# Optimization experiments

Measured on AMD Instinct MI355X. Metric: run time of the kernel, lower is better.

Reference implementation:

```python
import jax, jax.numpy as jnp
import numpy as np

N_STATE = 4      # d_state from CrossMambaFusionBlock(d_state=4)
DT_RANK = 48     # ceil(768/16), standard Mamba dt_rank='auto'
D_CONV = 4       # depthwise causal conv kernel size


def _ln(x, g, b):
    m = jnp.mean(x, axis=-1, keepdims=True)
    v = jnp.mean((x - m) ** 2, axis=-1, keepdims=True)
    return (x - m) * jax.lax.rsqrt(v + 1e-5) * g + b


def _dwconv1d(u, w, b):
    # u: (B,L,D); w: (D,1,K) depthwise causal conv along token dim L
    K = w.shape[-1]
    up = jnp.pad(jnp.transpose(u, (0, 2, 1)), ((0, 0), (0, 0), (K - 1, 0)))
    out = jax.lax.conv_general_dilated(up, w, (1,), 'VALID',
                                       feature_group_count=w.shape[0],
                                       dimension_numbers=('NCH', 'OIH', 'NCH'))
    return jnp.transpose(out, (0, 2, 1)) + b


def _pre(x, g, b, Win, Wconv, bconv, Wxp, Wdt, bdt):
    # LayerNorm -> in_proj -> depthwise conv + SiLU -> dt/B/C projections
    B_, H, W, C = x.shape
    xn = _ln(x, g, b).reshape(B_, H * W, C)
    u, z = jnp.split(xn @ Win, 2, axis=-1)              # (B,L,D) each
    u = jax.nn.silu(_dwconv1d(u, Wconv, bconv))
    dbl = u @ Wxp                                        # (B,L,R+2N)
    dtr, Bm, Cm = jnp.split(dbl, [DT_RANK, DT_RANK + N_STATE], axis=-1)
    dt = jax.nn.softplus(dtr @ Wdt + bdt)                # (B,L,D)
    return u, z, dt, Bm, Cm


def _selective_scan(u, dt, Alog, Bm, Cm, Dskip):
    # u, dt: (B,L,D); Alog: (D,N); Bm, Cm: (B,L,N)
    A = -jnp.exp(Alog)
    dA = jnp.exp(dt[..., None] * A)                      # (B,L,D,N) decay
    dBu = (dt * u)[..., None] * Bm[:, :, None, :]        # (B,L,D,N) input

    def comb(c1, c2):
        a1, h1 = c1
        a2, h2 = c2
        return a1 * a2, a2 * h1 + h2

    _, h = jax.lax.associative_scan(comb, (dA, dBu), axis=1)
    return jnp.einsum('bldn,bln->bld', h, Cm) + u * Dskip


def _forward(x1, x2,
             ln_g1, ln_b1, Win1, Wconv1, bconv1, Wxp1, Wdt1, bdt1, Alog1, Dskip1, Wout1,
             ln_g2, ln_b2, Win2, Wconv2, bconv2, Wxp2, Wdt2, bdt2, Alog2, Dskip2, Wout2):
    x1 = jnp.transpose(x1, (0, 2, 3, 1))  # BCHW -> BHWC (as in forward_features)
    x2 = jnp.transpose(x2, (0, 2, 3, 1))
    B_, H, W, C = x1.shape
    u1, z1, dt1, B1, C1 = _pre(x1, ln_g1, ln_b1, Win1, Wconv1, bconv1, Wxp1, Wdt1, bdt1)
    u2, z2, dt2, B2, C2 = _pre(x2, ln_g2, ln_b2, Win2, Wconv2, bconv2, Wxp2, Wdt2, bdt2)
    # Cross-modal fusion: each stream's SSM state is read out with the OTHER
    # stream's C projection (cross selective scan).
    y1 = _selective_scan(u1, dt1, Alog1, B1, C2, Dskip1)
    y2 = _selective_scan(u2, dt2, Alog2, B2, C1, Dskip2)
    o1 = ((y1 * jax.nn.silu(z1)) @ Wout1).reshape(B_, H, W, C)
    o2 = ((y2 * jax.nn.silu(z2)) @ Wout2).reshape(B_, H, W, C)
    return x1 + o1, x2 + o2


def setup_inputs():
    key = jax.random.key(0)
    ks = jax.random.split(key, 16)
    B_, C, H, W = 2, 768, 64, 64
    D = C  # d_inner (ssm_ratio = 1)

    def nrm(k, shape, s=0.02):
        return jax.random.normal(k, shape, jnp.float32) * s

    inp = {
        'x1': jax.random.normal(ks[0], (B_, C, H, W), jnp.float32),
        'x2': jax.random.normal(ks[1], (B_, C, H, W), jnp.float32),
    }
    for i, o in ((1, 2), (2, 8)):
        inp[f'ln_g{i}'] = jnp.ones((C,), jnp.float32)
        inp[f'ln_b{i}'] = jnp.zeros((C,), jnp.float32)
        inp[f'Win{i}'] = nrm(ks[o], (C, 2 * D))
        inp[f'Wconv{i}'] = nrm(ks[o + 1], (D, 1, D_CONV), 0.1)
        inp[f'bconv{i}'] = jnp.zeros((D,), jnp.float32)
        inp[f'Wxp{i}'] = nrm(ks[o + 2], (D, DT_RANK + 2 * N_STATE))
        inp[f'Wdt{i}'] = nrm(ks[o + 3], (DT_RANK, D), 0.05)
        inp[f'bdt{i}'] = jnp.full((D,), -4.6, jnp.float32)  # softplus -> dt ~ 0.01
        inp[f'Alog{i}'] = jnp.log(jnp.broadcast_to(
            jnp.arange(1, N_STATE + 1, dtype=jnp.float32), (D, N_STATE)))
        inp[f'Dskip{i}'] = jnp.ones((D,), jnp.float32)
        inp[f'Wout{i}'] = nrm(ks[o + 4], (D, C))
    return inp


def reference(x1, x2,
              ln_g1, ln_b1, Win1, Wconv1, bconv1, Wxp1, Wdt1, bdt1, Alog1, Dskip1, Wout1,
              ln_g2, ln_b2, Win2, Wconv2, bconv2, Wxp2, Wdt2, bdt2, Alog2, Dskip2, Wout2):
    return _forward(x1, x2,
                    ln_g1, ln_b1, Win1, Wconv1, bconv1, Wxp1, Wdt1, bdt1, Alog1, Dskip1, Wout1,
                    ln_g2, ln_b2, Win2, Wconv2, bconv2, Wxp2, Wdt2, bdt2, Alog2, Dskip2, Wout2)
```

## Files before the change

kernel.cpp:

```cpp
#include <hip/hip_runtime.h>
#include <cmath>

#define LDIM 4096
#define CDIM 768
#define BDIM 2
#define NST 4
#define RNK 48
#define CH 64
#define LC 64
#define NDT 1024

typedef short bf16x8 __attribute__((ext_vector_type(8)));
typedef float f32x4 __attribute__((ext_vector_type(4)));

__device__ __forceinline__ float sigmoidf_(float x) { return 1.f / (1.f + __expf(-x)); }

__device__ __forceinline__ unsigned short f2bf(float f) {
    unsigned int u = __float_as_uint(f);
    u += 0x7fffu + ((u >> 16) & 1u);
    return (unsigned short)(u >> 16);
}
__device__ __forceinline__ float bf2f(unsigned short us) {
    unsigned int u = ((unsigned int)us) << 16;
    return __uint_as_float(u);
}

__device__ __forceinline__ void llds16(const unsigned short* g, unsigned short* l) {
    __builtin_amdgcn_global_load_lds(
        (const __attribute__((address_space(1))) unsigned int*)g,
        (__attribute__((address_space(3))) unsigned int*)l, 16, 0, 0);
}

__global__ __launch_bounds__(256) void stats_kernel(const float* __restrict__ x0,
                                                    const float* __restrict__ x1,
                                                    float* __restrict__ stats)
{
    int blk = blockIdx.x;
    int s = blk >> 7;
    int b = (blk >> 6) & 1;
    int l0 = (blk & 63) * 64;
    int wave = threadIdx.x >> 6, lane = threadIdx.x & 63;
    const float* x = s ? x1 : x0;
    const float* xp = x + ((size_t)b * CDIM) * LDIM + l0 + lane;
    float sm = 0.f, sq = 0.f;
    int cbeg = wave * 192;
#pragma unroll
    for (int i0 = 0; i0 < 192; i0 += 16) {
        float v[16];
#pragma unroll
        for (int j = 0; j < 16; j++) v[j] = xp[(size_t)(cbeg + i0 + j) * LDIM];
#pragma unroll
        for (int j = 0; j < 16; j++) { sm += v[j]; sq += v[j] * v[j]; }
    }
    __shared__ float red[2][4][64];
    red[0][wave][lane] = sm;
    red[1][wave][lane] = sq;
    __syncthreads();
    if (wave == 0) {
        float s_ = red[0][0][lane] + red[0][1][lane] + red[0][2][lane] + red[0][3][lane];
        float q_ = red[1][0][lane] + red[1][1][lane] + red[1][2][lane] + red[1][3][lane];
        float m = s_ * (1.f / CDIM);
        float var = q_ * (1.f / CDIM) - m * m;
        int idx = s * 8192 + b * LDIM + l0 + lane;
        stats[2 * idx] = m;
        stats[2 * idx + 1] = rsqrtf(var + 1e-5f);
    }
}

__global__ __launch_bounds__(256) void transpose_ln_kernel(
    const float* __restrict__ x0, const float* __restrict__ x1,
    const float* __restrict__ g0, const float* __restrict__ bb0,
    const float* __restrict__ g1, const float* __restrict__ bb1,
    const float* __restrict__ stats,
    unsigned short* __restrict__ xnb0, unsigned short* __restrict__ xnb1,
    float* __restrict__ out)
{
    __shared__ float tile[64][65];
    int t = threadIdx.x;
    int c0 = blockIdx.x * 64, l0 = blockIdx.y * 64;
    int z = blockIdx.z;
    int s = z >> 1, b = z & 1;
    const float* x = s ? x1 : x0;
    const float* g = s ? g1 : g0;
    const float* bb = s ? bb1 : bb0;
    unsigned short* xnb = s ? xnb1 : xnb0;
    int tl = t & 63, tg = t >> 6;
#pragma unroll
    for (int i = 0; i < 16; i++) {
        int cl = tg * 16 + i;
        tile[cl][tl] = x[((size_t)(b * CDIM + c0 + cl)) * LDIM + l0 + tl];
    }
    __syncthreads();
    const size_t SZ = (size_t)BDIM * LDIM * CDIM;
#pragma unroll
    for (int i = 0; i < 16; i++) {
        int ll = tg * 16 + i;
        int l = l0 + ll, c = c0 + tl;
        float v = tile[tl][ll];
        int sidx = s * 8192 + b * LDIM + l;
        float m = stats[sidx * 2], rs = stats[sidx * 2 + 1];
        size_t o = ((size_t)(b * LDIM + l)) * CDIM + c;
        out[(size_t)s * SZ + o] = v;
        xnb[o] = f2bf((v - m) * rs * g[c] + bb[c]);
    }
}

__global__ __launch_bounds__(256) void wt_transpose_all(
    const float* __restrict__ Win0, const float* __restrict__ Win1,
    const float* __restrict__ Wout0, const float* __restrict__ Wout1,
    unsigned short* __restrict__ WinT0, unsigned short* __restrict__ WinT1,
    unsigned short* __restrict__ WoutT0, unsigned short* __restrict__ WoutT1)
{
    int z = blockIdx.z;
    const float* W = (z == 0) ? Win0 : (z == 1) ? Win1 : (z == 2) ? Wout0 : Wout1;
    unsigned short* Wt = (z == 0) ? WinT0 : (z == 1) ? WinT1 : (z == 2) ? WoutT0 : WoutT1;
    const int K = CDIM;
    const int N = (z < 2) ? 2 * CDIM : CDIM;
    if (blockIdx.x * 64 >= N) return;
    __shared__ float tile[64][65];
    int t = threadIdx.x;
    int n0 = blockIdx.x * 64, k0 = blockIdx.y * 64;
    int tn = t & 63, tg = t >> 6;
#pragma unroll
    for (int i = 0; i < 16; i++) {
        int kl = tg * 16 + i;
        tile[kl][tn] = W[(size_t)(k0 + kl) * N + n0 + tn];
    }
    __syncthreads();
#pragma unroll
    for (int i = 0; i < 16; i++) {
        int nl = tg * 16 + i;
        int k = k0 + tn, n = n0 + nl;
        Wt[(size_t)n * K + k] = f2bf(tile[tn][nl]);
    }
}

__global__ __launch_bounds__(256) void wcomb_kernel(
    const float* __restrict__ Wxp0, const float* __restrict__ Wdt0,
    const float* __restrict__ Wxp1, const float* __restrict__ Wdt1,
    unsigned short* __restrict__ W0, unsigned short* __restrict__ W1)
{
    int s = blockIdx.z;
    const float* Wxp = s ? Wxp1 : Wxp0;
    const float* Wdt = s ? Wdt1 : Wdt0;
    unsigned short* WcombT = s ? W1 : W0;
    int t = threadIdx.x;
    int k = blockIdx.x * 64 + (t & 63);
    int n0 = blockIdx.y * 64;
    float wx[RNK];
#pragma unroll
    for (int r = 0; r < RNK; r++) wx[r] = Wxp[k * 56 + r];
    for (int i = (t >> 6); i < 64; i += 4) {
        int n = n0 + i;
        float val;
        if (n < CDIM) {
            float acc = 0.f;
#pragma unroll
            for (int r = 0; r < RNK; r++) acc += wx[r] * Wdt[(size_t)r * CDIM + n];
            val = acc;
        } else if (n < CDIM + 8) {
            val = Wxp[k * 56 + RNK + (n - CDIM)];
        } else {
            val = 0.f;
        }
        WcombT[(size_t)n * CDIM + k] = f2bf(val);
    }
}

template <int NW>
__global__ __launch_bounds__(512, 2) void gemm_mfma(
    const unsigned short* __restrict__ A0, const unsigned short* __restrict__ A1,
    const unsigned short* __restrict__ Bt0, const unsigned short* __restrict__ Bt1,
    void* __restrict__ C0, void* __restrict__ C1, int ldc, int K, int epi,
    const float* __restrict__ bias0, const float* __restrict__ bias1,
    float* __restrict__ D0, float* __restrict__ D1)
{
    const unsigned short* A = blockIdx.z ? A1 : A0;
    const unsigned short* Bt = blockIdx.z ? Bt1 : Bt0;
    void* C = blockIdx.z ? C1 : C0;
    const float* bias = blockIdx.z ? bias1 : bias0;
    float* D = blockIdx.z ? D1 : D0;

    constexpr int BN = NW * 64;
    __shared__ unsigned short As[2][256 * 64];
    __shared__ unsigned short Bs[2][BN * 64];

    const int tid = threadIdx.x;
    const int wave = tid >> 6, lane = tid & 63;
    const int row0 = blockIdx.x * 256, col0 = blockIdx.y * BN;
    const int wm = (wave >> 2) * 128;
    const int wn = (wave & 3) * (NW * 16);
    f32x4 acc[8][NW] = {};

    const int rs = tid >> 3;
    const int kcg = (tid & 7) ^ (rs & 7);
    const unsigned short* gA = A + (size_t)(row0 + rs) * K + kcg * 8;
    const unsigned short* gB = Bt + (size_t)(col0 + rs) * K + kcg * 8;
    const size_t rK = (size_t)64 * K;
    const int fr = lane & 15, fc = lane >> 4;

    auto ldfrag = [&](const unsigned short* s, int row, int kc) -> bf16x8 {
        return *(const bf16x8*)&s[row * 64 + ((kc ^ (row & 7)) << 3)];
    };

#define GSTAGE(nb, kt)                                                  \
    do {                                                                \
        const unsigned short* a_ = gA + (size_t)(kt) * 64;              \
        const unsigned short* b_ = gB + (size_t)(kt) * 64;              \
        unsigned short* al = &As[nb][wave * 512];                       \
        unsigned short* bl = &Bs[nb][wave * 512];                       \
        _Pragma("unroll")                                               \
        for (int r_ = 0; r_ < 4; r_++) llds16(a_ + r_ * rK, al + r_ * 4096); \
        _Pragma("unroll")                                               \
        for (int r_ = 0; r_ < NW; r_++) llds16(b_ + r_ * rK, bl + r_ * 4096); \
    } while (0)

    const int NKT = K / 64;
    GSTAGE(0, 0);
    __builtin_amdgcn_s_waitcnt(0xF70);
    __builtin_amdgcn_s_barrier();

    for (int kt = 0; kt < NKT; kt++) {
        const int cur = kt & 1;
        const unsigned short* as = As[cur];
        const unsigned short* bs = Bs[cur];
        bf16x8 af[4], bfv[NW];

        if (kt + 1 < NKT) GSTAGE(cur ^ 1, kt + 1);
#pragma unroll
        for (int mi = 0; mi < 4; mi++) af[mi] = ldfrag(as, wm + mi * 16 + fr, fc);
#pragma unroll
        for (int nj = 0; nj < NW; nj++) bfv[nj] = ldfrag(bs, wn + nj * 16 + fr, fc);
        __builtin_amdgcn_s_barrier();
        __builtin_amdgcn_s_setprio(1);
#pragma unroll
        for (int mi = 0; mi < 4; mi++)
#pragma unroll
            for (int nj = 0; nj < NW; nj++)
                acc[mi][nj] = __builtin_amdgcn_mfma_f32_16x16x32_bf16(af[mi], bfv[nj], acc[mi][nj], 0, 0, 0);
        __builtin_amdgcn_s_setprio(0);
        __builtin_amdgcn_s_barrier();

#pragma unroll
        for (int mi = 0; mi < 4; mi++) af[mi] = ldfrag(as, wm + 64 + mi * 16 + fr, fc);
        __builtin_amdgcn_s_barrier();
        __builtin_amdgcn_s_setprio(1);
#pragma unroll
        for (int mi = 0; mi < 4; mi++)
#pragma unroll
            for (int nj = 0; nj < NW; nj++)
                acc[4 + mi][nj] = __builtin_amdgcn_mfma_f32_16x16x32_bf16(af[mi], bfv[nj], acc[4 + mi][nj], 0, 0, 0);
        __builtin_amdgcn_s_setprio(0);
        __builtin_amdgcn_s_barrier();

#pragma unroll
        for (int mi = 0; mi < 4; mi++) af[mi] = ldfrag(as, wm + mi * 16 + fr, 4 + fc);
#pragma unroll
        for (int nj = 0; nj < NW; nj++) bfv[nj] = ldfrag(bs, wn + nj * 16 + fr, 4 + fc);
        __builtin_amdgcn_s_barrier();
        __builtin_amdgcn_s_setprio(1);
#pragma unroll
        for (int mi = 0; mi < 4; mi++)
#pragma unroll
            for (int nj = 0; nj < NW; nj++)
                acc[mi][nj] = __builtin_amdgcn_mfma_f32_16x16x32_bf16(af[mi], bfv[nj], acc[mi][nj], 0, 0, 0);
        __builtin_amdgcn_s_setprio(0);
        __builtin_amdgcn_s_barrier();

#pragma unroll
        for (int mi = 0; mi < 4; mi++) af[mi] = ldfrag(as, wm + 64 + mi * 16 + fr, 4 + fc);
        __builtin_amdgcn_s_barrier();
        __builtin_amdgcn_s_setprio(1);
#pragma unroll
        for (int mi = 0; mi < 4; mi++)
#pragma unroll
            for (int nj = 0; nj < NW; nj++)
                acc[4 + mi][nj] = __builtin_amdgcn_mfma_f32_16x16x32_bf16(af[mi], bfv[nj], acc[4 + mi][nj], 0, 0, 0);
        __builtin_amdgcn_s_setprio(0);
        if (kt + 1 < NKT) __builtin_amdgcn_s_waitcnt(0xF70);
        __builtin_amdgcn_s_barrier();
    }
#undef GSTAGE

    const int cr = (lane >> 4) * 4, cc = lane & 15;
#pragma unroll
    for (int mi = 0; mi < 8; mi++)
#pragma unroll
        for (int nj = 0; nj < NW; nj++) {
            int col = col0 + wn + nj * 16 + cc;
#pragma unroll
            for (int r = 0; r < 4; r++) {
                int row = row0 + wm + mi * 16 + cr + r;
                float v = acc[mi][nj][r];
                if (epi == 1) {
                    float* Cf = (float*)C;
                    size_t o = (size_t)row * ldc + col;
                    Cf[o] = v + Cf[o];
                } else if (epi == 2) {
                    if (col < CDIM) {
                        v += bias[col];
                        v = (v > 20.f) ? v : __logf(1.f + __expf(v));
                        ((unsigned short*)C)[(size_t)row * ldc + col] = f2bf(v);
                    } else if (col < CDIM + 8) {
                        D[(size_t)row * 8 + (col - CDIM)] = v;
                    }
                } else {
                    ((unsigned short*)C)[(size_t)row * ldc + col] = f2bf(v);
                }
            }
        }
}

__global__ __launch_bounds__(256) void conv_silu_kernel(
    const unsigned short* __restrict__ uzb0, const unsigned short* __restrict__ uzb1,
    const float* __restrict__ w0, const float* __restrict__ bc0,
    const float* __restrict__ w1, const float* __restrict__ bc1,
    unsigned short* __restrict__ ub0, unsigned short* __restrict__ ub1)
{
    int s = blockIdx.y;
    const unsigned short* uzb = s ? uzb1 : uzb0;
    const float* w = s ? w1 : w0;
    const float* bc = s ? bc1 : bc0;
    unsigned short* ub = s ? ub1 : ub0;
    int idx = blockIdx.x * 256 + threadIdx.x;
    int d8 = (idx % 96) * 8;
    int bl = idx / 96;
    int l = bl & (LDIM - 1);

    float wr[8][4];
#pragma unroll
    for (int q = 0; q < 8; q++) {
        f32x4 wv = *(const f32x4*)&w[(d8 + q) * 4];
#pragma unroll
        for (int k = 0; k < 4; k++) wr[q][k] = wv[k];
    }
    float acc[8];
    f32x4 b0 = *(const f32x4*)&bc[d8];
    f32x4 b1 = *(const f32x4*)&bc[d8 + 4];
#pragma unroll
    for (int q = 0; q < 4; q++) { acc[q] = b0[q]; acc[4 + q] = b1[q]; }

#pragma unroll
    for (int k = 0; k < 4; k++) {
        int ls = l - 3 + k;
        if (ls >= 0) {
            bf16x8 uv = *(const bf16x8*)&uzb[(size_t)(bl - 3 + k) * (2 * CDIM) + d8];
#pragma unroll
            for (int q = 0; q < 8; q++)
                acc[q] += bf2f((unsigned short)uv[q]) * wr[q][k];
        }
    }
    bf16x8 ov;
#pragma unroll
    for (int q = 0; q < 8; q++) {
        float v = acc[q];
        ov[q] = (short)f2bf(v * sigmoidf_(v));
    }
    *(bf16x8*)&ub[(size_t)bl * CDIM + d8] = ov;
}

__global__ __launch_bounds__(256) void scan_phaseA(
    const unsigned short* __restrict__ u0, const unsigned short* __restrict__ dt0,
    const float* __restrict__ dbl0, const float* __restrict__ Alog0,
    const unsigned short* __restrict__ u1, const unsigned short* __restrict__ dt1,
    const float* __restrict__ dbl1, const float* __restrict__ Alog1,
    float* __restrict__ agg)
{
    int idx = blockIdx.x * 256 + threadIdx.x;
    int d = idx % CDIM;
    int t1 = idx / CDIM;
    int c = t1 % CH;
    int t2 = t1 / CH;
    int b = t2 & 1;
    int s = t2 >> 1;
    const unsigned short* u = s ? u1 : u0;
    const unsigned short* dt = s ? dt1 : dt0;
    const float* dbl = s ? dbl1 : dbl0;
    const float* Alog = s ? Alog1 : Alog0;
    float A[4];
#pragma unroll
    for (int n = 0; n < 4; n++) A[n] = -__expf(Alog[d * 4 + n]);
    float h[4] = {0, 0, 0, 0}, aa[4] = {1, 1, 1, 1};
    int rowb = b * LDIM + c * LC;
    for (int t = 0; t < LC; t++) {
        int row = rowb + t;
        float dtv = bf2f(dt[(size_t)row * CDIM + d]);
        float uv = bf2f(u[(size_t)row * CDIM + d]);
        float du = dtv * uv;
        const float* bm = dbl + (size_t)row * 8;
#pragma unroll
        for (int n = 0; n < 4; n++) {
            float dA = __expf(dtv * A[n]);
            h[n] = dA * h[n] + du * bm[n];
            aa[n] *= dA;
        }
    }
    float* o = agg + (size_t)idx * 8;
#pragma unroll
    for (int n = 0; n < 4; n++) { o[n] = aa[n]; o[4 + n] = h[n]; }
}

__global__ __launch_bounds__(256) void scan_phaseB(const float* __restrict__ agg,
                                                   float* __restrict__ hinit)
{
    int idx = blockIdx.x * 256 + threadIdx.x;
    int d = idx % CDIM;
    int sb = idx / CDIM;
    float st[4] = {0, 0, 0, 0};
    for (int c = 0; c < CH; c++) {
        size_t base = ((size_t)sb * CH + c) * CDIM + d;
        const float* a = agg + base * 8;
        float* hi = hinit + base * 4;
#pragma unroll
        for (int n = 0; n < 4; n++) hi[n] = st[n];
#pragma unroll
        for (int n = 0; n < 4; n++) st[n] = a[n] * st[n] + a[4 + n];
    }
}

__global__ __launch_bounds__(256) void scan_phaseC(
    const unsigned short* __restrict__ u0, const unsigned short* __restrict__ dt0,
    const unsigned short* __restrict__ uzb0, const float* __restrict__ dbl0,
    const float* __restrict__ Alog0, const float* __restrict__ Dsk0, unsigned short* __restrict__ g0,
    const unsigned short* __restrict__ u1, const unsigned short* __restrict__ dt1,
    const unsigned short* __restrict__ uzb1, const float* __restrict__ dbl1,
    const float* __restrict__ Alog1, const float* __restrict__ Dsk1, unsigned short* __restrict__ g1,
    const float* __restrict__ hinit)
{
    int idx = blockIdx.x * 256 + threadIdx.x;
    int d = idx % CDIM;
    int t1 = idx / CDIM;
    int c = t1 % CH;
    int t2 = t1 / CH;
    int b = t2 & 1;
    int s = t2 >> 1;
    const unsigned short* u = s ? u1 : u0;
    const unsigned short* dt = s ? dt1 : dt0;
    const unsigned short* uzb = s ? uzb1 : uzb0;
    const float* dbl = s ? dbl1 : dbl0;
    const float* dblO = s ? dbl0 : dbl1;
    const float* Alog = s ? Alog1 : Alog0;
    const float* Dsk = s ? Dsk1 : Dsk0;
    unsigned short* gated = s ? g1 : g0;
    float A[4];
#pragma unroll
    for (int n = 0; n < 4; n++) A[n] = -__expf(Alog[d * 4 + n]);
    float Dv = Dsk[d];
    float h[4];
    const float* hi = hinit + (size_t)idx * 4;
#pragma unroll
    for (int n = 0; n < 4; n++) h[n] = hi[n];
    int rowb = b * LDIM + c * LC;
    for (int t = 0; t < LC; t++) {
        int row = rowb + t;
        float dtv = bf2f(dt[(size_t)row * CDIM + d]);
        float uv = bf2f(u[(size_t)row * CDIM + d]);
        float du = dtv * uv;
        const float* bm = dbl + (size_t)row * 8;
        const float* cm = dblO + (size_t)row * 8 + 4;
        float y = 0.f;
#pragma unroll
        for (int n = 0; n < 4; n++) {
            float dA = __expf(dtv * A[n]);
            h[n] = dA * h[n] + du * bm[n];
            y += h[n] * cm[n];
        }
        y += uv * Dv;
        float zv = bf2f(uzb[(size_t)row * (2 * CDIM) + CDIM + d]);
        gated[(size_t)row * CDIM + d] = f2bf(y * (zv * sigmoidf_(zv)));
    }
}

extern "C" void kernel_launch(void* const* d_in, const int* in_sizes, int n_in,
                              void* d_out, int out_size, void* d_ws, size_t ws_size,
                              hipStream_t stream)
{
    const float* x[2] = {(const float*)d_in[0], (const float*)d_in[1]};
    const float *ln_g[2], *ln_b[2], *Win[2], *Wconv[2], *bconv[2], *Wxp[2],
        *Wdt[2], *bdt[2], *Alog[2], *Dskip[2], *Wout[2];
    for (int s = 0; s < 2; s++) {
        int base = 2 + s * 11;
        ln_g[s] = (const float*)d_in[base + 0];
        ln_b[s] = (const float*)d_in[base + 1];
        Win[s] = (const float*)d_in[base + 2];
        Wconv[s] = (const float*)d_in[base + 3];
        bconv[s] = (const float*)d_in[base + 4];
        Wxp[s] = (const float*)d_in[base + 5];
        Wdt[s] = (const float*)d_in[base + 6];
        bdt[s] = (const float*)d_in[base + 7];
        Alog[s] = (const float*)d_in[base + 8];
        Dskip[s] = (const float*)d_in[base + 9];
        Wout[s] = (const float*)d_in[base + 10];
    }

    const int M = BDIM * LDIM;
    char* base = (char*)d_ws;
    auto alloc = [&](size_t bytes) {
        char* p = base;
        base += (bytes + 255) & ~(size_t)255;
        return p;
    };
    unsigned short* uzb[2] = {(unsigned short*)alloc((size_t)M * 1536 * 2),
                              (unsigned short*)alloc((size_t)M * 1536 * 2)};
    unsigned short* dtb[2] = {(unsigned short*)alloc((size_t)M * CDIM * 2),
                              (unsigned short*)alloc((size_t)M * CDIM * 2)};
    unsigned short* ub[2] = {(unsigned short*)alloc((size_t)M * CDIM * 2),
                             (unsigned short*)alloc((size_t)M * CDIM * 2)};
    unsigned short* xnb[2] = {(unsigned short*)alloc((size_t)M * CDIM * 2),
                              (unsigned short*)alloc((size_t)M * CDIM * 2)};
    float* dbl[2] = {(float*)alloc((size_t)M * 8 * 4), (float*)alloc((size_t)M * 8 * 4)};
    unsigned short* WinT[2] = {(unsigned short*)alloc(1536 * 768 * 2),
                               (unsigned short*)alloc(1536 * 768 * 2)};
    unsigned short* WoutT[2] = {(unsigned short*)alloc(768 * 768 * 2),
                                (unsigned short*)alloc(768 * 768 * 2)};
    unsigned short* WcombT[2] = {(unsigned short*)alloc((size_t)NDT * 768 * 2),
                                 (unsigned short*)alloc((size_t)NDT * 768 * 2)};
    float* agg = (float*)alloc((size_t)2 * BDIM * CH * CDIM * 8 * 4);
    float* hinit = (float*)alloc((size_t)2 * BDIM * CH * CDIM * 4 * 4);
    float* stats = (float*)alloc((size_t)2 * M * 2 * 4);

    dim3 blk(256);
    dim3 blk512(512);
    const size_t SZ = (size_t)BDIM * LDIM * CDIM;

    stats_kernel<<<dim3(256), blk, 0, stream>>>(x[0], x[1], stats);
    transpose_ln_kernel<<<dim3(CDIM / 64, LDIM / 64, 4), blk, 0, stream>>>(
        x[0], x[1], ln_g[0], ln_b[0], ln_g[1], ln_b[1], stats, xnb[0], xnb[1], (float*)d_out);

    wt_transpose_all<<<dim3(1536 / 64, 768 / 64, 4), blk, 0, stream>>>(
        Win[0], Win[1], Wout[0], Wout[1], WinT[0], WinT[1], WoutT[0], WoutT[1]);
    wcomb_kernel<<<dim3(768 / 64, NDT / 64, 2), blk, 0, stream>>>(
        Wxp[0], Wdt[0], Wxp[1], Wdt[1], WcombT[0], WcombT[1]);

    gemm_mfma<3><<<dim3(M / 256, 1536 / 192, 2), blk512, 0, stream>>>(
        xnb[0], xnb[1], WinT[0], WinT[1], uzb[0], uzb[1], 2 * CDIM, CDIM, 3,
        nullptr, nullptr, nullptr, nullptr);

    conv_silu_kernel<<<dim3((M * CDIM / 8) / 256, 2), blk, 0, stream>>>(
        uzb[0], uzb[1], Wconv[0], bconv[0], Wconv[1], bconv[1], ub[0], ub[1]);

    gemm_mfma<4><<<dim3(M / 256, NDT / 256, 2), blk512, 0, stream>>>(
        ub[0], ub[1], WcombT[0], WcombT[1], dtb[0], dtb[1], CDIM, CDIM, 2,
        bdt[0], bdt[1], dbl[0], dbl[1]);

    scan_phaseA<<<dim3((2 * BDIM * CH * CDIM) / 256), blk, 0, stream>>>(
        ub[0], dtb[0], dbl[0], Alog[0], ub[1], dtb[1], dbl[1], Alog[1], agg);
    scan_phaseB<<<dim3((2 * BDIM * CDIM) / 256), blk, 0, stream>>>(agg, hinit);
    scan_phaseC<<<dim3((2 * BDIM * CH * CDIM) / 256), blk, 0, stream>>>(
        ub[0], dtb[0], uzb[0], dbl[0], Alog[0], Dskip[0], xnb[0],
        ub[1], dtb[1], uzb[1], dbl[1], Alog[1], Dskip[1], xnb[1], hinit);

    float* out = (float*)d_out;
    gemm_mfma<3><<<dim3(M / 256, CDIM / 192, 2), blk512, 0, stream>>>(
        xnb[0], xnb[1], WoutT[0], WoutT[1], out, out + SZ, CDIM, CDIM, 1,
        nullptr, nullptr, nullptr, nullptr);
}
```

Before: 490.1 us.

## Merge prep kernels, retile GEMM to 256x128, trim dt padding, vectorize LN loads

Merges the stats, weight-transpose and weight-combine kernels into one launch, which saves launch overhead. Replaces the templated GEMM, which had a 256xNW*64 tile and a barrier/setprio ping-pong schedule, with a fixed 256x128 tile using a 4x4 MFMA fragment per wave and a simpler loop with one barrier per k-step. The combined dt weight padding drops from 1024 to 896 columns, cutting wasted GEMM work. The LayerNorm transpose now loads input with float4 vectors. The simpler GEMM schedule may lose latency hiding and the smaller N tile reduces reuse of A.

After: 475.3 us. -3.0%, faster.

```diff
diff --git a/kernel.cpp b/kernel.cpp
--- a/kernel.cpp
+++ b/kernel.cpp
@@ -8,7 +8,7 @@
 #define RNK 48
 #define CH 64
 #define LC 64
-#define NDT 1024
+#define NDT 896
 
 typedef short bf16x8 __attribute__((ext_vector_type(8)));
 typedef float f32x4 __attribute__((ext_vector_type(4)));
@@ -31,39 +31,103 @@
         (__attribute__((address_space(3))) unsigned int*)l, 16, 0, 0);
 }
 
-__global__ __launch_bounds__(256) void stats_kernel(const float* __restrict__ x0,
-                                                    const float* __restrict__ x1,
-                                                    float* __restrict__ stats)
-{
-    int blk = blockIdx.x;
-    int s = blk >> 7;
-    int b = (blk >> 6) & 1;
-    int l0 = (blk & 63) * 64;
-    int wave = threadIdx.x >> 6, lane = threadIdx.x & 63;
-    const float* x = s ? x1 : x0;
-    const float* xp = x + ((size_t)b * CDIM) * LDIM + l0 + lane;
-    float sm = 0.f, sq = 0.f;
-    int cbeg = wave * 192;
-#pragma unroll
-    for (int i0 = 0; i0 < 192; i0 += 16) {
-        float v[16];
-#pragma unroll
-        for (int j = 0; j < 16; j++) v[j] = xp[(size_t)(cbeg + i0 + j) * LDIM];
-#pragma unroll
-        for (int j = 0; j < 16; j++) { sm += v[j]; sq += v[j] * v[j]; }
-    }
-    __shared__ float red[2][4][64];
-    red[0][wave][lane] = sm;
-    red[1][wave][lane] = sq;
-    __syncthreads();
-    if (wave == 0) {
-        float s_ = red[0][0][lane] + red[0][1][lane] + red[0][2][lane] + red[0][3][lane];
-        float q_ = red[1][0][lane] + red[1][1][lane] + red[1][2][lane] + red[1][3][lane];
-        float m = s_ * (1.f / CDIM);
-        float var = q_ * (1.f / CDIM) - m * m;
-        int idx = s * 8192 + b * LDIM + l0 + lane;
-        stats[2 * idx] = m;
-        stats[2 * idx + 1] = rsqrtf(var + 1e-5f);
+__global__ __launch_bounds__(256) void prep_kernel(
+    const float* __restrict__ x0, const float* __restrict__ x1, float* __restrict__ stats,
+    const float* __restrict__ Win0, const float* __restrict__ Win1,
+    const float* __restrict__ Wout0, const float* __restrict__ Wout1,
+    unsigned short* __restrict__ WinT0, unsigned short* __restrict__ WinT1,
+    unsigned short* __restrict__ WoutT0, unsigned short* __restrict__ WoutT1,
+    const float* __restrict__ Wxp0, const float* __restrict__ Wdt0,
+    const float* __restrict__ Wxp1, const float* __restrict__ Wdt1,
+    unsigned short* __restrict__ Wc0, unsigned short* __restrict__ Wc1)
+{
+    __shared__ float smem[64 * 65];
+    int bid = blockIdx.x;
+    int t = threadIdx.x;
+
+    if (bid < 256) {
+        int s = bid >> 7;
+        int b = (bid >> 6) & 1;
+        int l0 = (bid & 63) * 64;
+        int wave = t >> 6, lane = t & 63;
+        const float* x = s ? x1 : x0;
+        const float* xp = x + ((size_t)b * CDIM) * LDIM + l0 + lane;
+        float sm = 0.f, sq = 0.f;
+        int cbeg = wave * 192;
+#pragma unroll
+        for (int i0 = 0; i0 < 192; i0 += 16) {
+            float v[16];
+#pragma unroll
+            for (int j = 0; j < 16; j++) v[j] = xp[(size_t)(cbeg + i0 + j) * LDIM];
+#pragma unroll
+            for (int j = 0; j < 16; j++) { sm += v[j]; sq += v[j] * v[j]; }
+        }
+        float* red = smem;
+        red[(0 * 4 + wave) * 64 + lane] = sm;
+        red[(1 * 4 + wave) * 64 + lane] = sq;
+        __syncthreads();
+        if (wave == 0) {
+            float s_ = red[lane] + red[64 + lane] + red[128 + lane] + red[192 + lane];
+            float q_ = red[256 + lane] + red[320 + lane] + red[384 + lane] + red[448 + lane];
+            float m = s_ * (1.f / CDIM);
+            float var = q_ * (1.f / CDIM) - m * m;
+            int idx = s * 8192 + b * LDIM + l0 + lane;
+            stats[2 * idx] = m;
+            stats[2 * idx + 1] = rsqrtf(var + 1e-5f);
+        }
+        return;
+    }
+    if (bid < 1408) {
+        int b2 = bid - 256;
+        int bx = b2 % 24, by = (b2 / 24) % 12, z = b2 / 288;
+        const float* W = (z == 0) ? Win0 : (z == 1) ? Win1 : (z == 2) ? Wout0 : Wout1;
+        unsigned short* Wt = (z == 0) ? WinT0 : (z == 1) ? WinT1 : (z == 2) ? WoutT0 : WoutT1;
+        const int K = CDIM;
+        const int N = (z < 2) ? 2 * CDIM : CDIM;
+        if (bx * 64 >= N) return;
+        float (*tile)[65] = (float(*)[65])smem;
+        int n0 = bx * 64, k0 = by * 64;
+        int tn = t & 63, tg = t >> 6;
+#pragma unroll
+        for (int i = 0; i < 16; i++) {
+            int kl = tg * 16 + i;
+            tile[kl][tn] = W[(size_t)(k0 + kl) * N + n0 + tn];
+        }
+        __syncthreads();
+#pragma unroll
+        for (int i = 0; i < 16; i++) {
+            int nl = tg * 16 + i;
+            int k = k0 + tn, n = n0 + nl;
+            Wt[(size_t)n * K + k] = f2bf(tile[tn][nl]);
+        }
+        return;
+    }
+    {
+        int b3 = bid - 1408;
+        int bx = b3 % 12, by = (b3 / 12) % 14, s = b3 / 168;
+        const float* Wxp = s ? Wxp1 : Wxp0;
+        const float* Wdt = s ? Wdt1 : Wdt0;
+        unsigned short* WcombT = s ? Wc1 : Wc0;
+        int k = bx * 64 + (t & 63);
+        int n0 = by * 64;
+        float wx[RNK];
+#pragma unroll
+        for (int r = 0; r < RNK; r++) wx[r] = Wxp[k * 56 + r];
+        for (int i = (t >> 6); i < 64; i += 4) {
+            int n = n0 + i;
+            float val;
+            if (n < CDIM) {
+                float acc = 0.f;
+#pragma unroll
+                for (int r = 0; r < RNK; r++) acc += wx[r] * Wdt[(size_t)r * CDIM + n];
+                val = acc;
+            } else if (n < CDIM + 8) {
+                val = Wxp[k * 56 + RNK + (n - CDIM)];
+            } else {
+                val = 0.f;
+            }
+            WcombT[(size_t)n * CDIM + k] = f2bf(val);
+        }
     }
 }
 
@@ -84,14 +148,17 @@
     const float* g = s ? g1 : g0;
     const float* bb = s ? bb1 : bb0;
     unsigned short* xnb = s ? xnb1 : xnb0;
-    int tl = t & 63, tg = t >> 6;
-#pragma unroll
-    for (int i = 0; i < 16; i++) {
-        int cl = tg * 16 + i;
-        tile[cl][tl] = x[((size_t)(b * CDIM + c0 + cl)) * LDIM + l0 + tl];
+    int lane16 = t & 15, cg = t >> 4;
+#pragma unroll
+    for (int i = 0; i < 4; i++) {
+        int cl = cg + 16 * i;
+        f32x4 v = *(const f32x4*)&x[((size_t)(b * CDIM + c0 + cl)) * LDIM + l0 + lane16 * 4];
+#pragma unroll
+        for (int j = 0; j < 4; j++) tile[cl][lane16 * 4 + j] = v[j];
     }
     __syncthreads();
     const size_t SZ = (size_t)BDIM * LDIM * CDIM;
+    int tl = t & 63, tg = t >> 6;
 #pragma unroll
     for (int i = 0; i < 16; i++) {
         int ll = tg * 16 + i;
@@ -105,69 +172,6 @@
     }
 }
 
-__global__ __launch_bounds__(256) void wt_transpose_all(
-    const float* __restrict__ Win0, const float* __restrict__ Win1,
-    const float* __restrict__ Wout0, const float* __restrict__ Wout1,
-    unsigned short* __restrict__ WinT0, unsigned short* __restrict__ WinT1,
-    unsigned short* __restrict__ WoutT0, unsigned short* __restrict__ WoutT1)
-{
-    int z = blockIdx.z;
-    const float* W = (z == 0) ? Win0 : (z == 1) ? Win1 : (z == 2) ? Wout0 : Wout1;
-    unsigned short* Wt = (z == 0) ? WinT0 : (z == 1) ? WinT1 : (z == 2) ? WoutT0 : WoutT1;
-    const int K = CDIM;
-    const int N = (z < 2) ? 2 * CDIM : CDIM;
-    if (blockIdx.x * 64 >= N) return;
-    __shared__ float tile[64][65];
-    int t = threadIdx.x;
-    int n0 = blockIdx.x * 64, k0 = blockIdx.y * 64;
-    int tn = t & 63, tg = t >> 6;
-#pragma unroll
-    for (int i = 0; i < 16; i++) {
-        int kl = tg * 16 + i;
-        tile[kl][tn] = W[(size_t)(k0 + kl) * N + n0 + tn];
-    }
-    __syncthreads();
-#pragma unroll
-    for (int i = 0; i < 16; i++) {
-        int nl = tg * 16 + i;
-        int k = k0 + tn, n = n0 + nl;
-        Wt[(size_t)n * K + k] = f2bf(tile[tn][nl]);
-    }
-}
-
-__global__ __launch_bounds__(256) void wcomb_kernel(
-    const float* __restrict__ Wxp0, const float* __restrict__ Wdt0,
-    const float* __restrict__ Wxp1, const float* __restrict__ Wdt1,
-    unsigned short* __restrict__ W0, unsigned short* __restrict__ W1)
-{
-    int s = blockIdx.z;
-    const float* Wxp = s ? Wxp1 : Wxp0;
-    const float* Wdt = s ? Wdt1 : Wdt0;
-    unsigned short* WcombT = s ? W1 : W0;
-    int t = threadIdx.x;
-    int k = blockIdx.x * 64 + (t & 63);
-    int n0 = blockIdx.y * 64;
-    float wx[RNK];
-#pragma unroll
-    for (int r = 0; r < RNK; r++) wx[r] = Wxp[k * 56 + r];
-    for (int i = (t >> 6); i < 64; i += 4) {
-        int n = n0 + i;
-        float val;
-        if (n < CDIM) {
-            float acc = 0.f;
-#pragma unroll
-            for (int r = 0; r < RNK; r++) acc += wx[r] * Wdt[(size_t)r * CDIM + n];
-            val = acc;
-        } else if (n < CDIM + 8) {
-            val = Wxp[k * 56 + RNK + (n - CDIM)];
-        } else {
-            val = 0.f;
-        }
-        WcombT[(size_t)n * CDIM + k] = f2bf(val);
-    }
-}
-
-template <int NW>
 __global__ __launch_bounds__(512, 2) void gemm_mfma(
     const unsigned short* __restrict__ A0, const unsigned short* __restrict__ A1,
     const unsigned short* __restrict__ Bt0, const unsigned short* __restrict__ Bt1,
@@ -181,16 +185,15 @@
     const float* bias = blockIdx.z ? bias1 : bias0;
     float* D = blockIdx.z ? D1 : D0;
 
-    constexpr int BN = NW * 64;
     __shared__ unsigned short As[2][256 * 64];
-    __shared__ unsigned short Bs[2][BN * 64];
+    __shared__ unsigned short Bs[2][128 * 64];
 
     const int tid = threadIdx.x;
     const int wave = tid >> 6, lane = tid & 63;
-    const int row0 = blockIdx.x * 256, col0 = blockIdx.y * BN;
-    const int wm = (wave >> 2) * 128;
-    const int wn = (wave & 3) * (NW * 16);
-    f32x4 acc[8][NW] = {};
+    const int row0 = blockIdx.x * 256, col0 = blockIdx.y * 128;
+    const int wm = (wave >> 1) * 64;
+    const int wn = (wave & 1) * 64;
+    f32x4 acc[4][4] = {};
 
     const int rs = tid >> 3;
     const int kcg = (tid & 7) ^ (rs & 7);
@@ -203,16 +206,16 @@
         return *(const bf16x8*)&s[row * 64 + ((kc ^ (row & 7)) << 3)];
     };
 
-#define GSTAGE(nb, kt)                                                  \
-    do {                                                                \
-        const unsigned short* a_ = gA + (size_t)(kt) * 64;              \
-        const unsigned short* b_ = gB + (size_t)(kt) * 64;              \
-        unsigned short* al = &As[nb][wave * 512];                       \
-        unsigned short* bl = &Bs[nb][wave * 512];                       \
-        _Pragma("unroll")                                               \
+#define GSTAGE(nb, kt)                                                       \
+    do {                                                                     \
+        const unsigned short* a_ = gA + (size_t)(kt) * 64;                   \
+        const unsigned short* b_ = gB + (size_t)(kt) * 64;                   \
+        unsigned short* al = &As[nb][wave * 512];                            \
+        unsigned short* bl = &Bs[nb][wave * 512];                            \
+        _Pragma("unroll")                                                    \
         for (int r_ = 0; r_ < 4; r_++) llds16(a_ + r_ * rK, al + r_ * 4096); \
-        _Pragma("unroll")                                               \
-        for (int r_ = 0; r_ < NW; r_++) llds16(b_ + r_ * rK, bl + r_ * 4096); \
+        _Pragma("unroll")                                                    \
+        for (int r_ = 0; r_ < 2; r_++) llds16(b_ + r_ * rK, bl + r_ * 4096); \
     } while (0)
 
     const int NKT = K / 64;
@@ -222,71 +225,32 @@
 
     for (int kt = 0; kt < NKT; kt++) {
         const int cur = kt & 1;
+        if (kt + 1 < NKT) GSTAGE(cur ^ 1, kt + 1);
         const unsigned short* as = As[cur];
         const unsigned short* bs = Bs[cur];
-        bf16x8 af[4], bfv[NW];
-
-        if (kt + 1 < NKT) GSTAGE(cur ^ 1, kt + 1);
-#pragma unroll
-        for (int mi = 0; mi < 4; mi++) af[mi] = ldfrag(as, wm + mi * 16 + fr, fc);
-#pragma unroll
-        for (int nj = 0; nj < NW; nj++) bfv[nj] = ldfrag(bs, wn + nj * 16 + fr, fc);
+#pragma unroll
+        for (int ks = 0; ks < 2; ks++) {
+            bf16x8 af[4], bf[4];
+#pragma unroll
+            for (int mi = 0; mi < 4; mi++) af[mi] = ldfrag(as, wm + mi * 16 + fr, ks * 4 + fc);
+#pragma unroll
+            for (int nj = 0; nj < 4; nj++) bf[nj] = ldfrag(bs, wn + nj * 16 + fr, ks * 4 + fc);
+#pragma unroll
+            for (int mi = 0; mi < 4; mi++)
+#pragma unroll
+                for (int nj = 0; nj < 4; nj++)
+                    acc[mi][nj] = __builtin_amdgcn_mfma_f32_16x16x32_bf16(af[mi], bf[nj], acc[mi][nj], 0, 0, 0);
+        }
+        __builtin_amdgcn_s_waitcnt(0xF70);
         __builtin_amdgcn_s_barrier();
-        __builtin_amdgcn_s_setprio(1);
-#pragma unroll
-        for (int mi = 0; mi < 4; mi++)
-#pragma unroll
-            for (int nj = 0; nj < NW; nj++)
-                acc[mi][nj] = __builtin_amdgcn_mfma_f32_16x16x32_bf16(af[mi], bfv[nj], acc[mi][nj], 0, 0, 0);
-        __builtin_amdgcn_s_setprio(0);
-        __builtin_amdgcn_s_barrier();
-
-#pragma unroll
-        for (int mi = 0; mi < 4; mi++) af[mi] = ldfrag(as, wm + 64 + mi * 16 + fr, fc);
-        __builtin_amdgcn_s_barrier();
-        __builtin_amdgcn_s_setprio(1);
-#pragma unroll
-        for (int mi = 0; mi < 4; mi++)
-#pragma unroll
-            for (int nj = 0; nj < NW; nj++)
-                acc[4 + mi][nj] = __builtin_amdgcn_mfma_f32_16x16x32_bf16(af[mi], bfv[nj], acc[4 + mi][nj], 0, 0, 0);
-        __builtin_amdgcn_s_setprio(0);
-        __builtin_amdgcn_s_barrier();
-
-#pragma unroll
-        for (int mi = 0; mi < 4; mi++) af[mi] = ldfrag(as, wm + mi * 16 + fr, 4 + fc);
-#pragma unroll
-        for (int nj = 0; nj < NW; nj++) bfv[nj] = ldfrag(bs, wn + nj * 16 + fr, 4 + fc);
-        __builtin_amdgcn_s_barrier();
-        __builtin_amdgcn_s_setprio(1);
-#pragma unroll
-        for (int mi = 0; mi < 4; mi++)
-#pragma unroll
-            for (int nj = 0; nj < NW; nj++)
-                acc[mi][nj] = __builtin_amdgcn_mfma_f32_16x16x32_bf16(af[mi], bfv[nj], acc[mi][nj], 0, 0, 0);
-        __builtin_amdgcn_s_setprio(0);
-        __builtin_amdgcn_s_barrier();
-
-#pragma unroll
-        for (int mi = 0; mi < 4; mi++) af[mi] = ldfrag(as, wm + 64 + mi * 16 + fr, 4 + fc);
-        __builtin_amdgcn_s_barrier();
-        __builtin_amdgcn_s_setprio(1);
-#pragma unroll
-        for (int mi = 0; mi < 4; mi++)
-#pragma unroll
-            for (int nj = 0; nj < NW; nj++)
-                acc[4 + mi][nj] = __builtin_amdgcn_mfma_f32_16x16x32_bf16(af[mi], bfv[nj], acc[4 + mi][nj], 0, 0, 0);
-        __builtin_amdgcn_s_setprio(0);
-        if (kt + 1 < NKT) __builtin_amdgcn_s_waitcnt(0xF70);
-        __builtin_amdgcn_s_barrier();
     }
 #undef GSTAGE
 
     const int cr = (lane >> 4) * 4, cc = lane & 15;
 #pragma unroll
-    for (int mi = 0; mi < 8; mi++)
-#pragma unroll
-        for (int nj = 0; nj < NW; nj++) {
+    for (int mi = 0; mi < 4; mi++)
+#pragma unroll
+        for (int nj = 0; nj < 4; nj++) {
             int col = col0 + wn + nj * 16 + cc;
 #pragma unroll
             for (int r = 0; r < 4; r++) {
@@ -523,23 +487,22 @@
     dim3 blk512(512);
     const size_t SZ = (size_t)BDIM * LDIM * CDIM;
 
-    stats_kernel<<<dim3(256), blk, 0, stream>>>(x[0], x[1], stats);
+    prep_kernel<<<dim3(1744), blk, 0, stream>>>(
+        x[0], x[1], stats,
+        Win[0], Win[1], Wout[0], Wout[1], WinT[0], WinT[1], WoutT[0], WoutT[1],
+        Wxp[0], Wdt[0], Wxp[1], Wdt[1], WcombT[0], WcombT[1]);
+
     transpose_ln_kernel<<<dim3(CDIM / 64, LDIM / 64, 4), blk, 0, stream>>>(
         x[0], x[1], ln_g[0], ln_b[0], ln_g[1], ln_b[1], stats, xnb[0], xnb[1], (float*)d_out);
 
-    wt_transpose_all<<<dim3(1536 / 64, 768 / 64, 4), blk, 0, stream>>>(
-        Win[0], Win[1], Wout[0], Wout[1], WinT[0], WinT[1], WoutT[0], WoutT[1]);
-    wcomb_kernel<<<dim3(768 / 64, NDT / 64, 2), blk, 0, stream>>>(
-        Wxp[0], Wdt[0], Wxp[1], Wdt[1], WcombT[0], WcombT[1]);
-
-    gemm_mfma<3><<<dim3(M / 256, 1536 / 192, 2), blk512, 0, stream>>>(
+    gemm_mfma<<<dim3(M / 256, 1536 / 128, 2), blk512, 0, stream>>>(
         xnb[0], xnb[1], WinT[0], WinT[1], uzb[0], uzb[1], 2 * CDIM, CDIM, 3,
         nullptr, nullptr, nullptr, nullptr);
 
     conv_silu_kernel<<<dim3((M * CDIM / 8) / 256, 2), blk, 0, stream>>>(
         uzb[0], uzb[1], Wconv[0], bconv[0], Wconv[1], bconv[1], ub[0], ub[1]);
 
-    gemm_mfma<4><<<dim3(M / 256, NDT / 256, 2), blk512, 0, stream>>>(
+    gemm_mfma<<<dim3(M / 256, NDT / 128, 2), blk512, 0, stream>>>(
         ub[0], ub[1], WcombT[0], WcombT[1], dtb[0], dtb[1], CDIM, CDIM, 2,
         bdt[0], bdt[1], dbl[0], dbl[1]);
 
@@ -551,7 +514,7 @@
         ub[1], dtb[1], uzb[1], dbl[1], Alog[1], Dskip[1], xnb[1], hinit);
 
     float* out = (float*)d_out;
-    gemm_mfma<3><<<dim3(M / 256, CDIM / 192, 2), blk512, 0, stream>>>(
+    gemm_mfma<<<dim3(M / 256, CDIM / 128, 2), blk512, 0, stream>>>(
         xnb[0], xnb[1], WoutT[0], WoutT[1], out, out + SZ, CDIM, CDIM, 1,
         nullptr, nullptr, nullptr, nullptr);
 }
```
